# Kernel tuning notes

Measured on AMD Instinct MI355X. Metric: run time of the kernel, lower is better.

## Reference

```python
import jax, jax.numpy as jnp
import numpy as np

D_MODEL = 1024
H = 16
D_K = D_MODEL // H


def setup_inputs() -> dict:
    key = jax.random.key(0)
    ks = jax.random.split(key, 12)
    b, nq, nk = 2, 2048, 2048
    inp = {
        "queries": jax.random.normal(ks[0], (b, nq, D_MODEL), jnp.float32),
        "keys": jax.random.normal(ks[1], (b, nk, D_MODEL), jnp.float32),
        "values": jax.random.normal(ks[2], (b, nk, D_MODEL), jnp.float32),
        "query_mask": jax.random.uniform(ks[3], (b, nq), jnp.float32),
        "key_mask": jax.random.uniform(ks[4], (b, nk), jnp.float32),
        "attention_mask": jax.random.randint(ks[5], (b, 1, nq, nk), 0, 2).astype(bool),
        "attention_weights": jax.random.uniform(ks[6], (b, 1, nq, nk), jnp.float32),
        # Linear params init: normal(std=0.001) weights, zero bias (per init_weights)
        "Wq": 0.001 * jax.random.normal(ks[7], (D_MODEL, D_MODEL), jnp.float32),
        "Wk": 0.001 * jax.random.normal(ks[8], (D_MODEL, D_MODEL), jnp.float32),
        "Wv": 0.001 * jax.random.normal(ks[9], (D_MODEL, D_MODEL), jnp.float32),
        "Wo": 0.001 * jax.random.normal(ks[10], (D_MODEL, D_MODEL), jnp.float32),
        "bq": jnp.zeros((D_MODEL,), jnp.float32),
        "bk": jnp.zeros((D_MODEL,), jnp.float32),
        "bv": jnp.zeros((D_MODEL,), jnp.float32),
        "bo": jnp.zeros((D_MODEL,), jnp.float32),
    }
    return inp


def reference(queries, keys, values, query_mask, key_mask, attention_mask,
              attention_weights, Wq, Wk, Wv, Wo, bq, bk, bv, bo):
    b, nq, _ = queries.shape
    nk = keys.shape[1]
    # projections (torch Linear: x @ W.T + b)
    q = (queries @ Wq.T + bq).reshape(b, nq, H, D_K).transpose(0, 2, 1, 3)  # bhqd
    k = (keys @ Wk.T + bk).reshape(b, nk, H, D_K).transpose(0, 2, 1, 3)    # bhkd
    v = (values @ Wv.T + bv).reshape(b, nk, H, D_K).transpose(0, 2, 1, 3)  # bhkd
    # multiplicative per-token masks
    q = q * query_mask[:, None, :, None]
    k = k * key_mask[:, None, :, None]
    v = v * key_mask[:, None, :, None]
    att = jnp.einsum('bhqd,bhkd->bhqk', q, k) / np.sqrt(D_K).astype(np.float32)
    att = att * attention_weights
    att = jnp.where(attention_mask, -jnp.inf, att)
    att_softmax = jax.nn.softmax(att, axis=-1)
    # dropout is identity in eval/reference mode
    out = jnp.einsum('bhqk,bhkd->bhqd', att_softmax, v)
    out = out.transpose(0, 2, 1, 3).reshape(b, nq, H * D_K)
    out_final = out @ Wo.T + bo
    return (out_final, att_softmax)
```

## Files before the change

### kernel.cpp

```cpp
#include <hip/hip_runtime.h>

#define B2 2
#define NQ 2048
#define NK 2048
#define DM 1024
#define NH 16
#define DK 64
#define KC 64

typedef unsigned short u16;
typedef __attribute__((ext_vector_type(8))) short bf16x8;
typedef __attribute__((ext_vector_type(4))) float f32x4;

__device__ __forceinline__ u16 f2bf(float f) {
  unsigned u = __float_as_uint(f);
  u += 0x7FFFu + ((u >> 16) & 1u);
  return (u16)(u >> 16);
}
__device__ __forceinline__ float bf2f(u16 u) {
  return __uint_as_float(((unsigned)u) << 16);
}
__device__ __forceinline__ bf16x8 ld8f(const float* __restrict__ p) {
  const float4 a = *(const float4*)p;
  const float4 b = *(const float4*)(p + 4);
  bf16x8 v;
  v[0] = (short)f2bf(a.x); v[1] = (short)f2bf(a.y);
  v[2] = (short)f2bf(a.z); v[3] = (short)f2bf(a.w);
  v[4] = (short)f2bf(b.x); v[5] = (short)f2bf(b.y);
  v[6] = (short)f2bf(b.z); v[7] = (short)f2bf(b.w);
  return v;
}

#if __has_builtin(__builtin_amdgcn_exp2f)
#define EXP2F(x) __builtin_amdgcn_exp2f(x)
#else
#define EXP2F(x) exp2f(x)
#endif

#define MFMA(a, b, c) __builtin_amdgcn_mfma_f32_16x16x32_bf16(a, b, c, 0, 0, 0)

#define EXPC 0.18033688011112043f

template <bool AF32, bool WF32>
__device__ __forceinline__ void gemm_core(
    const void* __restrict__ Ap, const void* __restrict__ Wp,
    int tm, int tn, u16* As, u16* Bs, f32x4 acc[4][4]) {
  const int tid = threadIdx.x;
  const int lane = tid & 63;
  const int wid = tid >> 6;
  const int wm = (wid >> 1) * 64, wn = (wid & 1) * 64;
  const int cc = lane & 15, gg = lane >> 4;
  const int srow = tid >> 2, scol = 8 * (tid & 3);
  const size_t ra0 = (size_t)(tm + srow) * DM + scol;
  const size_t ra1 = (size_t)(tm + 64 + srow) * DM + scol;
  const size_t rb0 = (size_t)(tn + srow) * DM + scol;
  const size_t rb1 = (size_t)(tn + 64 + srow) * DM + scol;
  const float* Af = (const float*)Ap; const u16* Ab = (const u16*)Ap;
  const float* Wf = (const float*)Wp; const u16* Wb = (const u16*)Wp;
  const f32x4 Z4 = {0.f, 0.f, 0.f, 0.f};
#pragma unroll
  for (int i = 0; i < 4; i++)
#pragma unroll
    for (int j = 0; j < 4; j++) acc[i][j] = Z4;

#define LD_A(off) (AF32 ? ld8f(Af + (off)) : *(const bf16x8*)(Ab + (off)))
#define LD_W(off) (WF32 ? ld8f(Wf + (off)) : *(const bf16x8*)(Wb + (off)))
  *(bf16x8*)&As[tid * 8]        = LD_A(ra0);
  *(bf16x8*)&As[2048 + tid * 8] = LD_A(ra1);
  *(bf16x8*)&Bs[tid * 8]        = LD_W(rb0);
  *(bf16x8*)&Bs[2048 + tid * 8] = LD_W(rb1);

  int buf = 0;
  for (int kk = 0; kk < DM; kk += 32) {
    __syncthreads();
    const int o = buf * 4096;
    bf16x8 af[4], bv[4];
#pragma unroll
    for (int i = 0; i < 4; i++) af[i] = *(const bf16x8*)&As[o + (wm + i * 16 + cc) * 32 + 8 * gg];
#pragma unroll
    for (int i = 0; i < 4; i++) bv[i] = *(const bf16x8*)&Bs[o + (wn + i * 16 + cc) * 32 + 8 * gg];
    if (kk + 32 < DM) {
      const int p = (buf ^ 1) * 4096;
      *(bf16x8*)&As[p + tid * 8]        = LD_A(ra0 + kk + 32);
      *(bf16x8*)&As[p + 2048 + tid * 8] = LD_A(ra1 + kk + 32);
      *(bf16x8*)&Bs[p + tid * 8]        = LD_W(rb0 + kk + 32);
      *(bf16x8*)&Bs[p + 2048 + tid * 8] = LD_W(rb1 + kk + 32);
    }
#pragma unroll
    for (int mi = 0; mi < 4; mi++)
#pragma unroll
      for (int ni = 0; ni < 4; ni++) acc[mi][ni] = MFMA(af[mi], bv[ni], acc[mi][ni]);
    buf ^= 1;
  }
#undef LD_A
#undef LD_W
}

__global__ __launch_bounds__(256) void k_proj(
    const float* __restrict__ xq, const float* __restrict__ xk, const float* __restrict__ xv,
    const float* __restrict__ wq, const float* __restrict__ wk, const float* __restrict__ wv,
    const float* __restrict__ bq, const float* __restrict__ bk, const float* __restrict__ bv,
    const float* __restrict__ qmask, const float* __restrict__ kmask,
    u16* __restrict__ q_ws, u16* __restrict__ k_ws, u16* __restrict__ vT_ws,
    const float* __restrict__ attw, const int* __restrict__ amask, u16* __restrict__ fwo) {
  const int bid = blockIdx.x;
  if (bid >= 768) {
    for (int i = ((bid - 768) * 256 + threadIdx.x) * 8; i < NQ * NK * B2;
         i += 1024 * 256 * 8) {
#pragma unroll
      for (int hh = 0; hh < 2; hh++) {
        const float4 w = *(const float4*)(attw + i + 4 * hh);
        const int4 m = *(const int4*)(amask + i + 4 * hh);
        ushort4 o;
        o.x = m.x ? 0x7FC0 : f2bf(w.x);
        o.y = m.y ? 0x7FC0 : f2bf(w.y);
        o.z = m.z ? 0x7FC0 : f2bf(w.z);
        o.w = m.w ? 0x7FC0 : f2bf(w.w);
        *(ushort4*)(fwo + i + 4 * hh) = o;
      }
    }
    return;
  }
  __shared__ u16 As[2 * 4096];
  __shared__ u16 Bs[2 * 4096];
  const int swz = (bid & 7) * 96 + (bid >> 3);
  const int tm = (swz & 31) * 128;
  const int yz = swz >> 5;
  const int tn = (yz & 7) * 128;
  const int z = yz >> 3;
  const float* A = (z == 0) ? xq : (z == 1) ? xk : xv;
  const float* Wm = (z == 0) ? wq : (z == 1) ? wk : wv;
  const float* bias = (z == 0) ? bq : (z == 1) ? bk : bv;
  const float* rmask = (z == 0) ? qmask : kmask;
  f32x4 acc[4][4];
  gemm_core<true, true>(A, Wm, tm, tn, As, Bs, acc);

  const int lane = threadIdx.x & 63;
  const int wid = threadIdx.x >> 6;
  const int wm = (wid >> 1) * 64, wn = (wid & 1) * 64;
  const int cc = lane & 15, gg = lane >> 4;
  const int b = tm >> 11;
  const int tok0 = tm & 2047;
#pragma unroll
  for (int mi = 0; mi < 4; mi++) {
    const int rl = wm + mi * 16 + 4 * gg;
    float rm[4];
#pragma unroll
    for (int r = 0; r < 4; r++) rm[r] = rmask[b * NQ + tok0 + rl + r];
#pragma unroll
    for (int ni = 0; ni < 4; ni++) {
      const int col = tn + wn + ni * 16 + cc;
      const int h = col >> 6, d = col & 63;
      const float bs = bias[col];
      f32x4 a = acc[mi][ni];
      if (z <= 1) {
        u16* dst = ((z == 0) ? q_ws : k_ws) +
                   ((size_t)(b * NH + h) * NQ + tok0 + rl) * DK + d;
#pragma unroll
        for (int r = 0; r < 4; r++) dst[(size_t)r * DK] = f2bf((a[r] + bs) * rm[r]);
      } else {
        ushort4 pk;
        pk.x = f2bf((a[0] + bs) * rm[0]);
        pk.y = f2bf((a[1] + bs) * rm[1]);
        pk.z = f2bf((a[2] + bs) * rm[2]);
        pk.w = f2bf((a[3] + bs) * rm[3]);
        *(ushort4*)(vT_ws + ((size_t)(b * NH + h) * DK + d) * NK + tok0 + rl) = pk;
      }
    }
  }
}

__global__ __launch_bounds__(256) void k_attn(
    const u16* __restrict__ q_ws, const u16* __restrict__ k_ws, const u16* __restrict__ vT_ws,
    const u16* __restrict__ fw, float* __restrict__ att_out, u16* __restrict__ ctxb) {
  __shared__ u16 Ks[128][72];
  __shared__ u16 Ps[4][16][72];
  const int bh = blockIdx.y;
  const int b = bh >> 4, hh = bh & 15;
  const int qb = blockIdx.x * 64;
  const int tid = threadIdx.x, lane = tid & 63, wid = tid >> 6;
  const int cc = lane & 15, gg = lane >> 4;
  const int qr0 = qb + wid * 16;
  const u16* qp = q_ws + ((size_t)bh * NQ + qr0 + cc) * DK + 8 * gg;
  const bf16x8 aq0 = *(const bf16x8*)qp;
  const bf16x8 aq1 = *(const bf16x8*)(qp + 32);
  const u16* fwrow = fw + ((size_t)b * NQ + qr0 + cc) * NK;
  const f32x4 Z4 = {0.f, 0.f, 0.f, 0.f};
  const int sr = tid >> 3, sc = 8 * (tid & 7);

  float sum = 0.f;
  for (int kc = 0; kc < NK; kc += 128) {
#pragma unroll
    for (int i = 0; i < 4; i++)
      *(bf16x8*)&Ks[i * 32 + sr][sc] =
          *(const bf16x8*)(k_ws + ((size_t)bh * NK + kc + i * 32 + sr) * DK + sc);
    __syncthreads();
#pragma unroll
    for (int n = 0; n < 8; n++) {
      const bf16x8 k0 = *(const bf16x8*)&Ks[n * 16 + cc][8 * gg];
      const bf16x8 k1 = *(const bf16x8*)&Ks[n * 16 + cc][32 + 8 * gg];
      f32x4 acc = Z4;
      acc = MFMA(k0, aq0, acc);
      acc = MFMA(k1, aq1, acc);
      const int k0i = kc + n * 16 + 4 * gg;
      const ushort4 fv = *(const ushort4*)(fwrow + k0i);
      const float e0 = EXP2F(acc[0] * bf2f(fv.x) * EXPC);
      const float e1 = EXP2F(acc[1] * bf2f(fv.y) * EXPC);
      const float e2 = EXP2F(acc[2] * bf2f(fv.z) * EXPC);
      const float e3 = EXP2F(acc[3] * bf2f(fv.w) * EXPC);
      sum += (e0 == e0) ? e0 : 0.f;
      sum += (e1 == e1) ? e1 : 0.f;
      sum += (e2 == e2) ? e2 : 0.f;
      sum += (e3 == e3) ? e3 : 0.f;
    }
    __syncthreads();
  }
  sum += __shfl_xor(sum, 16);
  sum += __shfl_xor(sum, 32);
  const float rinv = (sum > 0.f) ? 1.0f / sum : 0.f;

  f32x4 o[4];
#pragma unroll
  for (int i = 0; i < 4; i++) o[i] = Z4;
  float* attrow = att_out + (size_t)bh * NQ * NK + (size_t)(qr0 + cc) * NK;

  for (int kc = 0; kc < NK; kc += KC) {
#pragma unroll
    for (int i = 0; i < 2; i++) {
      *(bf16x8*)&Ks[i * 32 + sr][sc] =
          *(const bf16x8*)(k_ws + ((size_t)bh * NK + kc + i * 32 + sr) * DK + sc);
      *(bf16x8*)&Ks[64 + i * 32 + sr][sc] =
          *(const bf16x8*)(vT_ws + ((size_t)bh * DK + i * 32 + sr) * NK + kc + sc);
    }
    __syncthreads();
#pragma unroll
    for (int n = 0; n < 4; n++) {
      const bf16x8 k0 = *(const bf16x8*)&Ks[n * 16 + cc][8 * gg];
      const bf16x8 k1 = *(const bf16x8*)&Ks[n * 16 + cc][32 + 8 * gg];
      f32x4 acc = Z4;
      acc = MFMA(k0, aq0, acc);
      acc = MFMA(k1, aq1, acc);
      const int k0i = kc + n * 16 + 4 * gg;
      const ushort4 fv = *(const ushort4*)(fwrow + k0i);
      const float e0 = EXP2F(acc[0] * bf2f(fv.x) * EXPC);
      const float e1 = EXP2F(acc[1] * bf2f(fv.y) * EXPC);
      const float e2 = EXP2F(acc[2] * bf2f(fv.z) * EXPC);
      const float e3 = EXP2F(acc[3] * bf2f(fv.w) * EXPC);
      f32x4 pv;
      pv.x = (e0 == e0) ? e0 * rinv : 0.f;
      pv.y = (e1 == e1) ? e1 * rinv : 0.f;
      pv.z = (e2 == e2) ? e2 * rinv : 0.f;
      pv.w = (e3 == e3) ? e3 * rinv : 0.f;
      __builtin_nontemporal_store(pv, (f32x4*)(attrow + k0i));
      ushort4 pk;
      pk.x = f2bf(pv.x); pk.y = f2bf(pv.y); pk.z = f2bf(pv.z); pk.w = f2bf(pv.w);
      *(ushort4*)&Ps[wid][cc][n * 16 + 4 * gg] = pk;
    }
    const bf16x8 pa0 = *(const bf16x8*)&Ps[wid][cc][8 * gg];
    const bf16x8 pa1 = *(const bf16x8*)&Ps[wid][cc][32 + 8 * gg];
#pragma unroll
    for (int nd = 0; nd < 4; nd++) {
      const bf16x8 vb0 = *(const bf16x8*)&Ks[64 + nd * 16 + cc][8 * gg];
      const bf16x8 vb1 = *(const bf16x8*)&Ks[64 + nd * 16 + cc][32 + 8 * gg];
      o[nd] = MFMA(pa0, vb0, o[nd]);
      o[nd] = MFMA(pa1, vb1, o[nd]);
    }
    __syncthreads();
  }
#pragma unroll
  for (int nd = 0; nd < 4; nd++)
#pragma unroll
    for (int r = 0; r < 4; r++)
      ctxb[((size_t)b * NQ + qr0 + 4 * gg + r) * DM + hh * 64 + nd * 16 + cc] = f2bf(o[nd][r]);
}

__global__ __launch_bounds__(256) void k_oproj(
    const u16* __restrict__ ctxb, const float* __restrict__ wo,
    const float* __restrict__ bo, float* __restrict__ outp) {
  __shared__ u16 As[2 * 4096];
  __shared__ u16 Bs[2 * 4096];
  const int bid = blockIdx.x;
  const int swz = ((bid & 7) << 5) + (bid >> 3);
  const int tm = (swz & 31) * 128;
  const int tn = (swz >> 5) * 128;
  f32x4 acc[4][4];
  gemm_core<false, true>(ctxb, wo, tm, tn, As, Bs, acc);
  const int lane = threadIdx.x & 63;
  const int wid = threadIdx.x >> 6;
  const int wm = (wid >> 1) * 64, wn = (wid & 1) * 64;
  const int cc = lane & 15, gg = lane >> 4;
#pragma unroll
  for (int mi = 0; mi < 4; mi++) {
    const int rl = tm + wm + mi * 16 + 4 * gg;
#pragma unroll
    for (int ni = 0; ni < 4; ni++) {
      const int col = tn + wn + ni * 16 + cc;
      const float bs = bo[col];
      f32x4 a = acc[mi][ni];
#pragma unroll
      for (int r = 0; r < 4; r++) outp[(size_t)(rl + r) * DM + col] = a[r] + bs;
    }
  }
}

extern "C" void kernel_launch(void* const* d_in, const int* in_sizes, int n_in,
                              void* d_out, int out_size, void* d_ws, size_t ws_size,
                              hipStream_t stream) {
  (void)in_sizes; (void)n_in; (void)out_size; (void)ws_size;
  const float* queries = (const float*)d_in[0];
  const float* keys    = (const float*)d_in[1];
  const float* values  = (const float*)d_in[2];
  const float* qmask   = (const float*)d_in[3];
  const float* kmask   = (const float*)d_in[4];
  const int*   amask   = (const int*)d_in[5];
  const float* attw    = (const float*)d_in[6];
  const float* Wq = (const float*)d_in[7];
  const float* Wk = (const float*)d_in[8];
  const float* Wv = (const float*)d_in[9];
  const float* Wo = (const float*)d_in[10];
  const float* bq = (const float*)d_in[11];
  const float* bk = (const float*)d_in[12];
  const float* bv = (const float*)d_in[13];
  const float* bo = (const float*)d_in[14];

  float* outf = (float*)d_out;
  float* att_out = outf + (size_t)4194304;

  char* p = (char*)d_ws;
  u16* q_ws  = (u16*)p; p += (size_t)4194304 * 2;
  u16* k_ws  = (u16*)p; p += (size_t)4194304 * 2;
  u16* vT_ws = (u16*)p; p += (size_t)4194304 * 2;
  u16* ctxb  = (u16*)p; p += (size_t)4194304 * 2;
  u16* fw    = (u16*)p; p += (size_t)8388608 * 2;

  k_proj<<<dim3(1792, 1, 1), 256, 0, stream>>>(queries, keys, values, Wq, Wk, Wv,
                                               bq, bk, bv, qmask, kmask,
                                               q_ws, k_ws, vT_ws, attw, amask, fw);
  k_attn<<<dim3(32, 32, 1), 256, 0, stream>>>(q_ws, k_ws, vT_ws, fw, att_out, ctxb);
  k_oproj<<<dim3(256, 1, 1), 256, 0, stream>>>(ctxb, Wo, bo, outf);
}
```

Before: 333.9 us.

## Process two query groups per attention block and fold exp scale into weights

Each attention workgroup now handles 128 query rows (two 16-row groups per wave) instead of 64, so every K/V tile loaded into shared memory is reused twice and the grid is halved. The softmax exponent constant is also multiplied into the bf16 attention-weight table during the projection kernel, which removes one multiply per score in both passes. The costs are higher register pressure from doubled accumulators and query fragments, fewer blocks (512) for occupancy, and slightly different rounding because the scale is applied before the bf16 conversion.

```diff
diff --git a/kernel.cpp b/kernel.cpp
--- a/kernel.cpp
+++ b/kernel.cpp
@@ -112,10 +112,10 @@
         const float4 w = *(const float4*)(attw + i + 4 * hh);
         const int4 m = *(const int4*)(amask + i + 4 * hh);
         ushort4 o;
-        o.x = m.x ? 0x7FC0 : f2bf(w.x);
-        o.y = m.y ? 0x7FC0 : f2bf(w.y);
-        o.z = m.z ? 0x7FC0 : f2bf(w.z);
-        o.w = m.w ? 0x7FC0 : f2bf(w.w);
+        o.x = m.x ? 0x7FC0 : f2bf(w.x * EXPC);
+        o.y = m.y ? 0x7FC0 : f2bf(w.y * EXPC);
+        o.z = m.z ? 0x7FC0 : f2bf(w.z * EXPC);
+        o.w = m.w ? 0x7FC0 : f2bf(w.w * EXPC);
         *(ushort4*)(fwo + i + 4 * hh) = o;
       }
     }
@@ -177,18 +177,28 @@
   __shared__ u16 Ps[4][16][72];
   const int bh = blockIdx.y;
   const int b = bh >> 4, hh = bh & 15;
-  const int qb = blockIdx.x * 64;
+  const int qb = blockIdx.x * 128;
   const int tid = threadIdx.x, lane = tid & 63, wid = tid >> 6;
   const int cc = lane & 15, gg = lane >> 4;
-  const int qr0 = qb + wid * 16;
-  const u16* qp = q_ws + ((size_t)bh * NQ + qr0 + cc) * DK + 8 * gg;
-  const bf16x8 aq0 = *(const bf16x8*)qp;
-  const bf16x8 aq1 = *(const bf16x8*)(qp + 32);
-  const u16* fwrow = fw + ((size_t)b * NQ + qr0 + cc) * NK;
   const f32x4 Z4 = {0.f, 0.f, 0.f, 0.f};
   const int sr = tid >> 3, sc = 8 * (tid & 7);
 
-  float sum = 0.f;
+  int qr[2];
+  qr[0] = qb + wid * 16;
+  qr[1] = qb + 64 + wid * 16;
+  bf16x8 aq0[2], aq1[2];
+  const u16* fwrow[2];
+  float* attrow[2];
+#pragma unroll
+  for (int g = 0; g < 2; g++) {
+    const u16* qp = q_ws + ((size_t)bh * NQ + qr[g] + cc) * DK + 8 * gg;
+    aq0[g] = *(const bf16x8*)qp;
+    aq1[g] = *(const bf16x8*)(qp + 32);
+    fwrow[g] = fw + ((size_t)b * NQ + qr[g] + cc) * NK;
+    attrow[g] = att_out + (size_t)bh * NQ * NK + (size_t)(qr[g] + cc) * NK;
+  }
+
+  float sum[2] = {0.f, 0.f};
   for (int kc = 0; kc < NK; kc += 128) {
 #pragma unroll
     for (int i = 0; i < 4; i++)
@@ -199,30 +209,38 @@
     for (int n = 0; n < 8; n++) {
       const bf16x8 k0 = *(const bf16x8*)&Ks[n * 16 + cc][8 * gg];
       const bf16x8 k1 = *(const bf16x8*)&Ks[n * 16 + cc][32 + 8 * gg];
-      f32x4 acc = Z4;
-      acc = MFMA(k0, aq0, acc);
-      acc = MFMA(k1, aq1, acc);
-      const int k0i = kc + n * 16 + 4 * gg;
-      const ushort4 fv = *(const ushort4*)(fwrow + k0i);
-      const float e0 = EXP2F(acc[0] * bf2f(fv.x) * EXPC);
-      const float e1 = EXP2F(acc[1] * bf2f(fv.y) * EXPC);
-      const float e2 = EXP2F(acc[2] * bf2f(fv.z) * EXPC);
-      const float e3 = EXP2F(acc[3] * bf2f(fv.w) * EXPC);
-      sum += (e0 == e0) ? e0 : 0.f;
-      sum += (e1 == e1) ? e1 : 0.f;
-      sum += (e2 == e2) ? e2 : 0.f;
-      sum += (e3 == e3) ? e3 : 0.f;
-    }
-    __syncthreads();
-  }
-  sum += __shfl_xor(sum, 16);
-  sum += __shfl_xor(sum, 32);
-  const float rinv = (sum > 0.f) ? 1.0f / sum : 0.f;
-
-  f32x4 o[4];
-#pragma unroll
-  for (int i = 0; i < 4; i++) o[i] = Z4;
-  float* attrow = att_out + (size_t)bh * NQ * NK + (size_t)(qr0 + cc) * NK;
+#pragma unroll
+      for (int g = 0; g < 2; g++) {
+        f32x4 acc = Z4;
+        acc = MFMA(k0, aq0[g], acc);
+        acc = MFMA(k1, aq1[g], acc);
+        const ushort4 fv = *(const ushort4*)(fwrow[g] + kc + n * 16 + 4 * gg);
+        const float e0 = EXP2F(acc[0] * bf2f(fv.x));
+        const float e1 = EXP2F(acc[1] * bf2f(fv.y));
+        const float e2 = EXP2F(acc[2] * bf2f(fv.z));
+        const float e3 = EXP2F(acc[3] * bf2f(fv.w));
+        sum[g] += (e0 == e0) ? e0 : 0.f;
+        sum[g] += (e1 == e1) ? e1 : 0.f;
+        sum[g] += (e2 == e2) ? e2 : 0.f;
+        sum[g] += (e3 == e3) ? e3 : 0.f;
+      }
+    }
+    __syncthreads();
+  }
+  float rinv[2];
+#pragma unroll
+  for (int g = 0; g < 2; g++) {
+    float s = sum[g];
+    s += __shfl_xor(s, 16);
+    s += __shfl_xor(s, 32);
+    rinv[g] = (s > 0.f) ? 1.0f / s : 0.f;
+  }
+
+  f32x4 o[2][4];
+#pragma unroll
+  for (int g = 0; g < 2; g++)
+#pragma unroll
+    for (int i = 0; i < 4; i++) o[g][i] = Z4;
 
   for (int kc = 0; kc < NK; kc += KC) {
 #pragma unroll
@@ -234,44 +252,50 @@
     }
     __syncthreads();
 #pragma unroll
-    for (int n = 0; n < 4; n++) {
-      const bf16x8 k0 = *(const bf16x8*)&Ks[n * 16 + cc][8 * gg];
-      const bf16x8 k1 = *(const bf16x8*)&Ks[n * 16 + cc][32 + 8 * gg];
-      f32x4 acc = Z4;
-      acc = MFMA(k0, aq0, acc);
-      acc = MFMA(k1, aq1, acc);
-      const int k0i = kc + n * 16 + 4 * gg;
-      const ushort4 fv = *(const ushort4*)(fwrow + k0i);
-      const float e0 = EXP2F(acc[0] * bf2f(fv.x) * EXPC);
-      const float e1 = EXP2F(acc[1] * bf2f(fv.y) * EXPC);
-      const float e2 = EXP2F(acc[2] * bf2f(fv.z) * EXPC);
-      const float e3 = EXP2F(acc[3] * bf2f(fv.w) * EXPC);
-      f32x4 pv;
-      pv.x = (e0 == e0) ? e0 * rinv : 0.f;
-      pv.y = (e1 == e1) ? e1 * rinv : 0.f;
-      pv.z = (e2 == e2) ? e2 * rinv : 0.f;
-      pv.w = (e3 == e3) ? e3 * rinv : 0.f;
-      __builtin_nontemporal_store(pv, (f32x4*)(attrow + k0i));
-      ushort4 pk;
-      pk.x = f2bf(pv.x); pk.y = f2bf(pv.y); pk.z = f2bf(pv.z); pk.w = f2bf(pv.w);
-      *(ushort4*)&Ps[wid][cc][n * 16 + 4 * gg] = pk;
-    }
-    const bf16x8 pa0 = *(const bf16x8*)&Ps[wid][cc][8 * gg];
-    const bf16x8 pa1 = *(const bf16x8*)&Ps[wid][cc][32 + 8 * gg];
-#pragma unroll
-    for (int nd = 0; nd < 4; nd++) {
-      const bf16x8 vb0 = *(const bf16x8*)&Ks[64 + nd * 16 + cc][8 * gg];
-      const bf16x8 vb1 = *(const bf16x8*)&Ks[64 + nd * 16 + cc][32 + 8 * gg];
-      o[nd] = MFMA(pa0, vb0, o[nd]);
-      o[nd] = MFMA(pa1, vb1, o[nd]);
-    }
-    __syncthreads();
-  }
-#pragma unroll
-  for (int nd = 0; nd < 4; nd++)
-#pragma unroll
-    for (int r = 0; r < 4; r++)
-      ctxb[((size_t)b * NQ + qr0 + 4 * gg + r) * DM + hh * 64 + nd * 16 + cc] = f2bf(o[nd][r]);
+    for (int g = 0; g < 2; g++) {
+#pragma unroll
+      for (int n = 0; n < 4; n++) {
+        const bf16x8 k0 = *(const bf16x8*)&Ks[n * 16 + cc][8 * gg];
+        const bf16x8 k1 = *(const bf16x8*)&Ks[n * 16 + cc][32 + 8 * gg];
+        f32x4 acc = Z4;
+        acc = MFMA(k0, aq0[g], acc);
+        acc = MFMA(k1, aq1[g], acc);
+        const int k0i = kc + n * 16 + 4 * gg;
+        const ushort4 fv = *(const ushort4*)(fwrow[g] + k0i);
+        const float e0 = EXP2F(acc[0] * bf2f(fv.x));
+        const float e1 = EXP2F(acc[1] * bf2f(fv.y));
+        const float e2 = EXP2F(acc[2] * bf2f(fv.z));
+        const float e3 = EXP2F(acc[3] * bf2f(fv.w));
+        f32x4 pv;
+        pv.x = (e0 == e0) ? e0 * rinv[g] : 0.f;
+        pv.y = (e1 == e1) ? e1 * rinv[g] : 0.f;
+        pv.z = (e2 == e2) ? e2 * rinv[g] : 0.f;
+        pv.w = (e3 == e3) ? e3 * rinv[g] : 0.f;
+        __builtin_nontemporal_store(pv, (f32x4*)(attrow[g] + k0i));
+        ushort4 pk;
+        pk.x = f2bf(pv.x); pk.y = f2bf(pv.y); pk.z = f2bf(pv.z); pk.w = f2bf(pv.w);
+        *(ushort4*)&Ps[wid][cc][n * 16 + 4 * gg] = pk;
+      }
+      const bf16x8 pa0 = *(const bf16x8*)&Ps[wid][cc][8 * gg];
+      const bf16x8 pa1 = *(const bf16x8*)&Ps[wid][cc][32 + 8 * gg];
+#pragma unroll
+      for (int nd = 0; nd < 4; nd++) {
+        const bf16x8 vb0 = *(const bf16x8*)&Ks[64 + nd * 16 + cc][8 * gg];
+        const bf16x8 vb1 = *(const bf16x8*)&Ks[64 + nd * 16 + cc][32 + 8 * gg];
+        o[g][nd] = MFMA(pa0, vb0, o[g][nd]);
+        o[g][nd] = MFMA(pa1, vb1, o[g][nd]);
+      }
+    }
+    __syncthreads();
+  }
+#pragma unroll
+  for (int g = 0; g < 2; g++)
+#pragma unroll
+    for (int nd = 0; nd < 4; nd++)
+#pragma unroll
+      for (int r = 0; r < 4; r++)
+        ctxb[((size_t)b * NQ + qr[g] + 4 * gg + r) * DM + hh * 64 + nd * 16 + cc] =
+            f2bf(o[g][nd][r]);
 }
 
 __global__ __launch_bounds__(256) void k_oproj(
@@ -336,6 +360,6 @@
   k_proj<<<dim3(1792, 1, 1), 256, 0, stream>>>(queries, keys, values, Wq, Wk, Wv,
                                                bq, bk, bv, qmask, kmask,
                                                q_ws, k_ws, vT_ws, attw, amask, fw);
-  k_attn<<<dim3(32, 32, 1), 256, 0, stream>>>(q_ws, k_ws, vT_ws, fw, att_out, ctxb);
+  k_attn<<<dim3(16, 32, 1), 256, 0, stream>>>(q_ws, k_ws, vT_ws, fw, att_out, ctxb);
   k_oproj<<<dim3(256, 1, 1), 256, 0, stream>>>(ctxb, Wo, bo, outf);
 }
```

Measured after the change: 484.0 us. 1.45x slower.

## Prefetch K/V tiles into registers and fold softmax scale into exponent

Applied to the files above, without the earlier changes.

Both attention passes now load the next K (and V^T) tile from global memory into registers while the current tile's MFMAs and exponentials run, then write it to LDS after the barrier. This hides global load latency behind compute. The EXPC scale is folded into the precomputed bf16 weight/mask tensor, and the normalisation becomes a log2 offset inside an fma before exp2 instead of a multiply after it. Costs are extra registers for the staged tiles and a small change in rounding, since EXPC is applied before bf16 conversion.

```diff
diff --git a/kernel.cpp b/kernel.cpp
--- a/kernel.cpp
+++ b/kernel.cpp
@@ -112,10 +112,10 @@
         const float4 w = *(const float4*)(attw + i + 4 * hh);
         const int4 m = *(const int4*)(amask + i + 4 * hh);
         ushort4 o;
-        o.x = m.x ? 0x7FC0 : f2bf(w.x);
-        o.y = m.y ? 0x7FC0 : f2bf(w.y);
-        o.z = m.z ? 0x7FC0 : f2bf(w.z);
-        o.w = m.w ? 0x7FC0 : f2bf(w.w);
+        o.x = m.x ? 0x7FC0 : f2bf(w.x * EXPC);
+        o.y = m.y ? 0x7FC0 : f2bf(w.y * EXPC);
+        o.z = m.z ? 0x7FC0 : f2bf(w.z * EXPC);
+        o.w = m.w ? 0x7FC0 : f2bf(w.w * EXPC);
         *(ushort4*)(fwo + i + 4 * hh) = o;
       }
     }
@@ -187,14 +187,23 @@
   const u16* fwrow = fw + ((size_t)b * NQ + qr0 + cc) * NK;
   const f32x4 Z4 = {0.f, 0.f, 0.f, 0.f};
   const int sr = tid >> 3, sc = 8 * (tid & 7);
+  const u16* kb = k_ws + (size_t)bh * NK * DK;
+  const u16* vb = vT_ws + (size_t)bh * DK * NK;
 
   float sum = 0.f;
+  bf16x8 st[4];
+#pragma unroll
+  for (int i = 0; i < 4; i++) st[i] = *(const bf16x8*)(kb + (size_t)(i * 32 + sr) * DK + sc);
+#pragma unroll
+  for (int i = 0; i < 4; i++) *(bf16x8*)&Ks[i * 32 + sr][sc] = st[i];
   for (int kc = 0; kc < NK; kc += 128) {
-#pragma unroll
-    for (int i = 0; i < 4; i++)
-      *(bf16x8*)&Ks[i * 32 + sr][sc] =
-          *(const bf16x8*)(k_ws + ((size_t)bh * NK + kc + i * 32 + sr) * DK + sc);
-    __syncthreads();
+    __syncthreads();
+    const bool more = (kc + 128) < NK;
+    if (more) {
+#pragma unroll
+      for (int i = 0; i < 4; i++)
+        st[i] = *(const bf16x8*)(kb + (size_t)(kc + 128 + i * 32 + sr) * DK + sc);
+    }
 #pragma unroll
     for (int n = 0; n < 8; n++) {
       const bf16x8 k0 = *(const bf16x8*)&Ks[n * 16 + cc][8 * gg];
@@ -202,37 +211,52 @@
       f32x4 acc = Z4;
       acc = MFMA(k0, aq0, acc);
       acc = MFMA(k1, aq1, acc);
-      const int k0i = kc + n * 16 + 4 * gg;
-      const ushort4 fv = *(const ushort4*)(fwrow + k0i);
-      const float e0 = EXP2F(acc[0] * bf2f(fv.x) * EXPC);
-      const float e1 = EXP2F(acc[1] * bf2f(fv.y) * EXPC);
-      const float e2 = EXP2F(acc[2] * bf2f(fv.z) * EXPC);
-      const float e3 = EXP2F(acc[3] * bf2f(fv.w) * EXPC);
+      const ushort4 fv = *(const ushort4*)(fwrow + kc + n * 16 + 4 * gg);
+      const float e0 = EXP2F(acc[0] * bf2f(fv.x));
+      const float e1 = EXP2F(acc[1] * bf2f(fv.y));
+      const float e2 = EXP2F(acc[2] * bf2f(fv.z));
+      const float e3 = EXP2F(acc[3] * bf2f(fv.w));
       sum += (e0 == e0) ? e0 : 0.f;
       sum += (e1 == e1) ? e1 : 0.f;
       sum += (e2 == e2) ? e2 : 0.f;
       sum += (e3 == e3) ? e3 : 0.f;
     }
     __syncthreads();
+    if (more) {
+#pragma unroll
+      for (int i = 0; i < 4; i++) *(bf16x8*)&Ks[i * 32 + sr][sc] = st[i];
+    }
   }
   sum += __shfl_xor(sum, 16);
   sum += __shfl_xor(sum, 32);
-  const float rinv = (sum > 0.f) ? 1.0f / sum : 0.f;
+  const float lg2r = (sum > 0.f) ? -__log2f(sum) : -__builtin_inff();
 
   f32x4 o[4];
 #pragma unroll
   for (int i = 0; i < 4; i++) o[i] = Z4;
   float* attrow = att_out + (size_t)bh * NQ * NK + (size_t)(qr0 + cc) * NK;
 
+  bf16x8 stk[2], stv[2];
+#pragma unroll
+  for (int i = 0; i < 2; i++) {
+    stk[i] = *(const bf16x8*)(kb + (size_t)(i * 32 + sr) * DK + sc);
+    stv[i] = *(const bf16x8*)(vb + (size_t)(i * 32 + sr) * NK + sc);
+  }
+#pragma unroll
+  for (int i = 0; i < 2; i++) {
+    *(bf16x8*)&Ks[i * 32 + sr][sc] = stk[i];
+    *(bf16x8*)&Ks[64 + i * 32 + sr][sc] = stv[i];
+  }
   for (int kc = 0; kc < NK; kc += KC) {
-#pragma unroll
-    for (int i = 0; i < 2; i++) {
-      *(bf16x8*)&Ks[i * 32 + sr][sc] =
-          *(const bf16x8*)(k_ws + ((size_t)bh * NK + kc + i * 32 + sr) * DK + sc);
-      *(bf16x8*)&Ks[64 + i * 32 + sr][sc] =
-          *(const bf16x8*)(vT_ws + ((size_t)bh * DK + i * 32 + sr) * NK + kc + sc);
-    }
-    __syncthreads();
+    __syncthreads();
+    const bool more = (kc + KC) < NK;
+    if (more) {
+#pragma unroll
+      for (int i = 0; i < 2; i++) {
+        stk[i] = *(const bf16x8*)(kb + (size_t)(kc + KC + i * 32 + sr) * DK + sc);
+        stv[i] = *(const bf16x8*)(vb + (size_t)(i * 32 + sr) * NK + kc + KC + sc);
+      }
+    }
 #pragma unroll
     for (int n = 0; n < 4; n++) {
       const bf16x8 k0 = *(const bf16x8*)&Ks[n * 16 + cc][8 * gg];
@@ -242,15 +266,15 @@
       acc = MFMA(k1, aq1, acc);
       const int k0i = kc + n * 16 + 4 * gg;
       const ushort4 fv = *(const ushort4*)(fwrow + k0i);
-      const float e0 = EXP2F(acc[0] * bf2f(fv.x) * EXPC);
-      const float e1 = EXP2F(acc[1] * bf2f(fv.y) * EXPC);
-      const float e2 = EXP2F(acc[2] * bf2f(fv.z) * EXPC);
-      const float e3 = EXP2F(acc[3] * bf2f(fv.w) * EXPC);
+      const float e0 = EXP2F(fmaf(acc[0], bf2f(fv.x), lg2r));
+      const float e1 = EXP2F(fmaf(acc[1], bf2f(fv.y), lg2r));
+      const float e2 = EXP2F(fmaf(acc[2], bf2f(fv.z), lg2r));
+      const float e3 = EXP2F(fmaf(acc[3], bf2f(fv.w), lg2r));
       f32x4 pv;
-      pv.x = (e0 == e0) ? e0 * rinv : 0.f;
-      pv.y = (e1 == e1) ? e1 * rinv : 0.f;
-      pv.z = (e2 == e2) ? e2 * rinv : 0.f;
-      pv.w = (e3 == e3) ? e3 * rinv : 0.f;
+      pv.x = (e0 == e0) ? e0 : 0.f;
+      pv.y = (e1 == e1) ? e1 : 0.f;
+      pv.z = (e2 == e2) ? e2 : 0.f;
+      pv.w = (e3 == e3) ? e3 : 0.f;
       __builtin_nontemporal_store(pv, (f32x4*)(attrow + k0i));
       ushort4 pk;
       pk.x = f2bf(pv.x); pk.y = f2bf(pv.y); pk.z = f2bf(pv.z); pk.w = f2bf(pv.w);
@@ -266,6 +290,13 @@
       o[nd] = MFMA(pa1, vb1, o[nd]);
     }
     __syncthreads();
+    if (more) {
+#pragma unroll
+      for (int i = 0; i < 2; i++) {
+        *(bf16x8*)&Ks[i * 32 + sr][sc] = stk[i];
+        *(bf16x8*)&Ks[64 + i * 32 + sr][sc] = stv[i];
+      }
+    }
   }
 #pragma unroll
   for (int nd = 0; nd < 4; nd++)
```

Result: slower. 361.8 us (+8.3%).
